# Kernel tuning notes

Measured on AMD Instinct MI355X. Metric: run time of the kernel, lower is better.

## Reference

```python
import jax, jax.numpy as jnp
import numpy as np

WIN_LEN = 400
WIN_INC = 100
FFT_LEN = 512
EPSILON = float(np.finfo(np.float32).eps)


def _make_kernel():
    # periodic (fftbins=True) hamming window, matching scipy.signal.get_window
    n = np.arange(WIN_LEN)
    window = 0.54 - 0.46 * np.cos(2.0 * np.pi * n / WIN_LEN)
    # direct-DFT basis: rfft of identity, truncated to win_len taps
    fourier_basis = np.fft.rfft(np.eye(FFT_LEN))[:WIN_LEN]          # [win_len, fft_len//2+1]
    kernel = np.concatenate([fourier_basis.real, fourier_basis.imag], axis=1).T  # [2*(fft//2+1), win_len]
    kernel = kernel * window                                        # window applied per tap
    return kernel[:, None, :].astype(np.float32)                    # [514, 1, 400] (OIH)


def setup_inputs() -> dict:
    key = jax.random.key(0)
    inputs = jax.random.normal(key, (16, 160000), dtype=jnp.float32)  # [B, L] waveform
    weight = jnp.asarray(_make_kernel())                              # fixed DFT buffer
    return {"inputs": inputs, "weight": weight}


def reference(inputs, weight):
    pad = WIN_LEN - WIN_INC  # 300
    x = inputs[:, None, :]                                   # [B, 1, L]
    x = jnp.pad(x, ((0, 0), (0, 0), (pad, pad)))             # symmetric pad, as in F.pad
    out = jax.lax.conv_general_dilated(
        x, weight,
        window_strides=(WIN_INC,),
        padding='VALID',
        dimension_numbers=('NCH', 'OIH', 'NCH'),
    )                                                        # [B, 514, T]
    r, i = jnp.split(out, 2, axis=1)                         # real / imag halves [B, 257, T]
    mags = jnp.sqrt(jnp.clip(r * r + i * i, EPSILON))
    phase = jnp.arctan2(i + EPSILON, r + EPSILON)
    return mags, phase
```

## Files before the change

### kernel.cpp

```cpp
#include <hip/hip_runtime.h>
#include <math.h>


#define BATCH 16
#define NSAMP 160000
#define NF 257
#define NT 1603
#define KLEN 400
#define INC 100
#define PADL 300
#define EPSF 1.1920928955078125e-7f
#define TAU 1e-2f

#define FPB 16
#define ZSTR 258
#define XSPAN ((FPB - 1) * INC + KLEN)
#define NTB ((NT + FPB - 1) / FPB)

__device__ __forceinline__ float2 cmul(float2 a, float2 b) {
  return make_float2(a.x * b.x - a.y * b.y, a.x * b.y + a.y * b.x);
}

__device__ __forceinline__ void fft16_dif(float2* a) {
  const float C1 = 0.92387953251128674f;
  const float S1 = 0.38268343236508978f;
  const float R2 = 0.70710678118654752f;
  {
    const float2 W[8] = {{1.f, 0.f},  {C1, -S1},  {R2, -R2},  {S1, -C1},
                         {0.f, -1.f}, {-S1, -C1}, {-R2, -R2}, {-C1, -S1}};
    #pragma unroll
    for (int j = 0; j < 8; ++j) {
      float2 u = a[j], v = a[j + 8];
      a[j] = make_float2(u.x + v.x, u.y + v.y);
      float2 d = make_float2(u.x - v.x, u.y - v.y);
      a[j + 8] = cmul(d, W[j]);
    }
  }
  {
    const float2 W[4] = {{1.f, 0.f}, {R2, -R2}, {0.f, -1.f}, {-R2, -R2}};
    #pragma unroll
    for (int h = 0; h < 16; h += 8)
      #pragma unroll
      for (int j = 0; j < 4; ++j) {
        float2 u = a[h + j], v = a[h + j + 4];
        a[h + j] = make_float2(u.x + v.x, u.y + v.y);
        float2 d = make_float2(u.x - v.x, u.y - v.y);
        a[h + j + 4] = cmul(d, W[j]);
      }
  }
  #pragma unroll
  for (int q = 0; q < 16; q += 4) {
    float2 u0 = a[q], v0 = a[q + 2];
    a[q] = make_float2(u0.x + v0.x, u0.y + v0.y);
    a[q + 2] = make_float2(u0.x - v0.x, u0.y - v0.y);
    float2 u1 = a[q + 1], v1 = a[q + 3];
    a[q + 1] = make_float2(u1.x + v1.x, u1.y + v1.y);
    float2 d = make_float2(u1.x - v1.x, u1.y - v1.y);
    a[q + 3] = make_float2(d.y, -d.x);
  }
  #pragma unroll
  for (int q = 0; q < 16; q += 2) {
    float2 u = a[q], v = a[q + 1];
    a[q] = make_float2(u.x + v.x, u.y + v.y);
    a[q + 1] = make_float2(u.x - v.x, u.y - v.y);
  }
}

__device__ __forceinline__ void emit_fp(float rr, float ii, int ff,
                                        const float* __restrict__ w,
                                        const float* xf,
                                        float* __restrict__ out,
                                        long o, long plane) {
  float ie = ii + EPSF, re = rr + EPSF;
  if (fabsf(ie) < TAU && re < TAU) {
    const float* wr = w + (long)ff * KLEN;
    const float* wi = w + (long)(257 + ff) * KLEN;
    float r2 = 0.f, i2 = 0.f;
    for (int k = 0; k < KLEN; ++k) {
      float xv = xf[k];
      r2 = fmaf(wr[k], xv, r2);
      i2 = fmaf(wi[k], xv, i2);
    }
    rr = r2; ii = i2;
  }
  out[o] = sqrtf(fmaxf(rr * rr + ii * ii, EPSF));
  out[o + plane] = atan2f(ii + EPSF, rr + EPSF);
}

__global__ __launch_bounds__(256, 3)
void stft_fft4(const float* __restrict__ x, const float* __restrict__ w,
               float* __restrict__ out) {
  __shared__ float2 Z[FPB * ZSTR];
  __shared__ float2 tw[132];
  __shared__ float2 tw256[256];
  __shared__ __align__(16) float xs[XSPAN];
  __shared__ __align__(16) float win[KLEN];

  const int tid = threadIdx.x;
  const int t0 = blockIdx.x * FPB;
  const int b = blockIdx.y;
  const int tl = tid & 15;
  const int th = tid >> 4;

  const long xb = (long)b * NSAMP;
  const int base = t0 * INC - PADL;
  for (int r = 0; r < 2; ++r) {
    int i4 = r * 256 + tid;
    if (4 * i4 < XSPAN) {
      int g = base + 4 * i4;
      float4 v;
      if (g >= 0 && g + 3 < NSAMP) {
        v = *(const float4*)(x + xb + g);
      } else {
        v.x = (g + 0 >= 0 && g + 0 < NSAMP) ? x[xb + g + 0] : 0.f;
        v.y = (g + 1 >= 0 && g + 1 < NSAMP) ? x[xb + g + 1] : 0.f;
        v.z = (g + 2 >= 0 && g + 2 < NSAMP) ? x[xb + g + 2] : 0.f;
        v.w = (g + 3 >= 0 && g + 3 < NSAMP) ? x[xb + g + 3] : 0.f;
      }
      *(float4*)&xs[4 * i4] = v;
    }
  }
  if (tid < KLEN / 4) {
    *(float4*)&win[4 * tid] = *(const float4*)(w + 4 * tid);
  }
  {
    double a = (double)tid * (6.283185307179586476925286766559 / 256.0);
    tw256[tid] = make_float2((float)cos(a), (float)(-sin(a)));
  }
  if (tid < 132) {
    double a = (double)tid * (6.283185307179586476925286766559 / 512.0);
    tw[tid] = make_float2((float)cos(a), (float)(-sin(a)));
  }
  __syncthreads();

  float2 a[16];
  const float* xf = &xs[tl * INC];
  #pragma unroll
  for (int n1 = 0; n1 < 12; ++n1) {
    int n = 32 * n1 + 2 * th;
    float2 xv = *(const float2*)&xf[n];
    float2 wv = *(const float2*)&win[n];
    a[n1] = make_float2(xv.x * wv.x, xv.y * wv.y);
  }
  {
    int n = 384 + 2 * th;
    if (n < KLEN) {
      float2 xv = *(const float2*)&xf[n];
      float2 wv = *(const float2*)&win[n];
      a[12] = make_float2(xv.x * wv.x, xv.y * wv.y);
    } else {
      a[12] = make_float2(0.f, 0.f);
    }
  }
  a[13] = a[14] = a[15] = make_float2(0.f, 0.f);

  fft16_dif(a);

  static const int BR[16] = {0, 8, 4, 12, 2, 10, 6, 14,
                             1, 9, 5, 13, 3, 11, 7, 15};
  float2* Zf = Z + tl * ZSTR;
  #pragma unroll
  for (int r = 0; r < 16; ++r) {
    const int k1 = BR[r];
    float2 v = (k1 == 0) ? a[r] : cmul(a[r], tw256[th * k1]);
    Zf[th * 16 + k1] = v;
  }
  __syncthreads();

  float2 g[16];
  #pragma unroll
  for (int n2 = 0; n2 < 16; ++n2) g[n2] = Zf[n2 * 16 + th];
  fft16_dif(g);
  #pragma unroll
  for (int r = 0; r < 16; ++r) {
    const int k2 = BR[r];
    Zf[16 * k2 + th] = g[r];
  }
  __syncthreads();

  const long plane = (long)BATCH * NF * NT;
  const long pb = (long)b * NF * NT;
  for (int r = 0; r < 9; ++r) {
    int tau = r * 256 + tid;
    if (tau < FPB * 129) {
      int t = tau & 15;
      int p = tau >> 4;
      float2* Zt = Z + t * ZSTR;
      float2 z0 = Zt[p];
      float2 z1 = Zt[(256 - p) & 255];
      float2 ze = make_float2(0.5f * (z0.x + z1.x), 0.5f * (z0.y - z1.y));
      float2 zo = make_float2(0.5f * (z0.y + z1.y), 0.5f * (z1.x - z0.x));
      float2 T = tw[p];
      float2 tz = cmul(zo, T);
      float2 ya = make_float2(ze.x + tz.x, ze.y + tz.y);
      float2 yb = make_float2(ze.x - tz.x, tz.y - ze.y);
      int tt = t0 + t;
      if (tt < NT) {
        const float* xfr = &xs[t * INC];
        emit_fp(ya.x, ya.y, p, w, xfr, out, pb + (long)p * NT + tt, plane);
        if (p == 0) {
          emit_fp(yb.x, 0.f, 256, w, xfr, out, pb + (long)256 * NT + tt, plane);
        } else {
          emit_fp(yb.x, yb.y, 256 - p, w, xfr, out,
                  pb + (long)(256 - p) * NT + tt, plane);
        }
      }
    }
  }
}

extern "C" void kernel_launch(void* const* d_in, const int* in_sizes, int n_in,
                              void* d_out, int out_size, void* d_ws, size_t ws_size,
                              hipStream_t stream) {
  const float* x = (const float*)d_in[0];
  const float* w = (const float*)d_in[1];
  float* out = (float*)d_out;

  dim3 grid(NTB, BATCH);
  stft_fft4<<<grid, dim3(256), 0, stream>>>(x, w, out);
}
```

Measured before the change: 156.0 us.

## Drop shared input staging, add fast atan2, swizzle LDS, remap blocks across XCDs

The input waveform is no longer staged in shared memory. Windowed samples are read straight from global memory, which cuts LDS use and raises the launch-bounds occupancy target from 3 to 4. The software atan2f is replaced by a polynomial approximation built on the hardware reciprocal. FFT scratch accesses use a rotated slot index to avoid LDS bank conflicts. Twiddles are computed with cospif/sinpif in float instead of double, and block indices are remapped so contiguous time tiles land on the same XCD. The polynomial atan2 adds approximation error near the tolerance boundary, and the direct global reads rely on caching for reuse across overlapping frames.

```diff
diff --git a/kernel.cpp b/kernel.cpp
--- a/kernel.cpp
+++ b/kernel.cpp
@@ -14,8 +14,8 @@
 
 #define FPB 16
 #define ZSTR 258
-#define XSPAN ((FPB - 1) * INC + KLEN)
 #define NTB ((NT + FPB - 1) / FPB)
+#define SLOT(j, k) (16 * (j) + (((k) + (j)) & 15))
 
 __device__ __forceinline__ float2 cmul(float2 a, float2 b) {
   return make_float2(a.x * b.x - a.y * b.y, a.x * b.y + a.y * b.x);
@@ -66,9 +66,26 @@
   }
 }
 
+__device__ __forceinline__ float fast_atan2(float y, float x) {
+  float ax = fabsf(x), ay = fabsf(y);
+  float mx = fmaxf(ax, ay), mn = fminf(ax, ay);
+  float t = mn * __builtin_amdgcn_rcpf(fmaxf(mx, 1e-37f));
+  float s = t * t;
+  float p = fmaf(s, -0.01172120f, 0.05265332f);
+  p = fmaf(s, p, -0.11643287f);
+  p = fmaf(s, p, 0.19354346f);
+  p = fmaf(s, p, -0.33262347f);
+  p = fmaf(s, p, 0.99997726f);
+  float r = t * p;
+  if (ay > ax) r = 1.57079632679489662f - r;
+  if (x < 0.f) r = 3.14159265358979324f - r;
+  return (y < 0.f) ? -r : r;
+}
+
 __device__ __forceinline__ void emit_fp(float rr, float ii, int ff,
                                         const float* __restrict__ w,
-                                        const float* xf,
+                                        const float* __restrict__ x,
+                                        long xb, int gb,
                                         float* __restrict__ out,
                                         long o, long plane) {
   float ie = ii + EPSF, re = rr + EPSF;
@@ -77,80 +94,64 @@
     const float* wi = w + (long)(257 + ff) * KLEN;
     float r2 = 0.f, i2 = 0.f;
     for (int k = 0; k < KLEN; ++k) {
-      float xv = xf[k];
+      int g = gb + k;
+      float xv = (g >= 0 && g < NSAMP) ? x[xb + g] : 0.f;
       r2 = fmaf(wr[k], xv, r2);
       i2 = fmaf(wi[k], xv, i2);
     }
     rr = r2; ii = i2;
   }
   out[o] = sqrtf(fmaxf(rr * rr + ii * ii, EPSF));
-  out[o + plane] = atan2f(ii + EPSF, rr + EPSF);
-}
-
-__global__ __launch_bounds__(256, 3)
-void stft_fft4(const float* __restrict__ x, const float* __restrict__ w,
+  out[o + plane] = fast_atan2(ii + EPSF, rr + EPSF);
+}
+
+__global__ __launch_bounds__(256, 4)
+void stft_fft8(const float* __restrict__ x, const float* __restrict__ w,
                float* __restrict__ out) {
   __shared__ float2 Z[FPB * ZSTR];
   __shared__ float2 tw[132];
   __shared__ float2 tw256[256];
-  __shared__ __align__(16) float xs[XSPAN];
   __shared__ __align__(16) float win[KLEN];
 
   const int tid = threadIdx.x;
-  const int t0 = blockIdx.x * FPB;
   const int b = blockIdx.y;
   const int tl = tid & 15;
   const int th = tid >> 4;
 
+  const int u = blockIdx.x;
+  const int xcd = u & 7;
+  const int tb = ((xcd < 5) ? xcd * 13 : 65 + (xcd - 5) * 12) + (u >> 3);
+  const int t0 = tb * FPB;
+
   const long xb = (long)b * NSAMP;
-  const int base = t0 * INC - PADL;
-  for (int r = 0; r < 2; ++r) {
-    int i4 = r * 256 + tid;
-    if (4 * i4 < XSPAN) {
-      int g = base + 4 * i4;
-      float4 v;
-      if (g >= 0 && g + 3 < NSAMP) {
-        v = *(const float4*)(x + xb + g);
-      } else {
-        v.x = (g + 0 >= 0 && g + 0 < NSAMP) ? x[xb + g + 0] : 0.f;
-        v.y = (g + 1 >= 0 && g + 1 < NSAMP) ? x[xb + g + 1] : 0.f;
-        v.z = (g + 2 >= 0 && g + 2 < NSAMP) ? x[xb + g + 2] : 0.f;
-        v.w = (g + 3 >= 0 && g + 3 < NSAMP) ? x[xb + g + 3] : 0.f;
-      }
-      *(float4*)&xs[4 * i4] = v;
-    }
-  }
   if (tid < KLEN / 4) {
     *(float4*)&win[4 * tid] = *(const float4*)(w + 4 * tid);
   }
   {
-    double a = (double)tid * (6.283185307179586476925286766559 / 256.0);
-    tw256[tid] = make_float2((float)cos(a), (float)(-sin(a)));
+    float a = (float)tid * (1.0f / 128.0f);
+    tw256[tid] = make_float2(cospif(a), -sinpif(a));
   }
   if (tid < 132) {
-    double a = (double)tid * (6.283185307179586476925286766559 / 512.0);
-    tw[tid] = make_float2((float)cos(a), (float)(-sin(a)));
+    float a = (float)tid * (1.0f / 256.0f);
+    tw[tid] = make_float2(cospif(a), -sinpif(a));
   }
   __syncthreads();
 
   float2 a[16];
-  const float* xf = &xs[tl * INC];
-  #pragma unroll
-  for (int n1 = 0; n1 < 12; ++n1) {
+  const int gb1 = (t0 + tl) * INC - PADL;
+  #pragma unroll
+  for (int n1 = 0; n1 < 13; ++n1) {
     int n = 32 * n1 + 2 * th;
-    float2 xv = *(const float2*)&xf[n];
-    float2 wv = *(const float2*)&win[n];
-    a[n1] = make_float2(xv.x * wv.x, xv.y * wv.y);
-  }
-  {
-    int n = 384 + 2 * th;
+    float2 zv = make_float2(0.f, 0.f);
     if (n < KLEN) {
-      float2 xv = *(const float2*)&xf[n];
-      float2 wv = *(const float2*)&win[n];
-      a[12] = make_float2(xv.x * wv.x, xv.y * wv.y);
-    } else {
-      a[12] = make_float2(0.f, 0.f);
-    }
+      int g = gb1 + n;
+      if (g >= 0 && g < NSAMP) {
+        float2 xv = *(const float2*)(x + xb + g);
+        float2 wv = *(const float2*)&win[n];
+        zv = make_float2(xv.x * wv.x, xv.y * wv.y);
+      }
+    }
+    a[n1] = zv;
   }
   a[13] = a[14] = a[15] = make_float2(0.f, 0.f);
 
@@ -163,18 +164,20 @@
   for (int r = 0; r < 16; ++r) {
     const int k1 = BR[r];
     float2 v = (k1 == 0) ? a[r] : cmul(a[r], tw256[th * k1]);
-    Zf[th * 16 + k1] = v;
+    Zf[SLOT(th, k1)] = v;
   }
   __syncthreads();
 
-  float2 g[16];
-  #pragma unroll
-  for (int n2 = 0; n2 < 16; ++n2) g[n2] = Zf[n2 * 16 + th];
-  fft16_dif(g);
-  #pragma unroll
-  for (int r = 0; r < 16; ++r) {
-    const int k2 = BR[r];
-    Zf[16 * k2 + th] = g[r];
+  {
+    float2 g[16];
+    #pragma unroll
+    for (int n2 = 0; n2 < 16; ++n2) g[n2] = Zf[SLOT(n2, th)];
+    fft16_dif(g);
+    #pragma unroll
+    for (int r = 0; r < 16; ++r) {
+      const int k2 = BR[r];
+      Zf[SLOT(k2, th)] = g[r];
+    }
   }
   __syncthreads();
 
@@ -183,25 +186,28 @@
   for (int r = 0; r < 9; ++r) {
     int tau = r * 256 + tid;
     if (tau < FPB * 129) {
-      int t = tau & 15;
+      int t16 = tau & 15;
       int p = tau >> 4;
-      float2* Zt = Z + t * ZSTR;
-      float2 z0 = Zt[p];
-      float2 z1 = Zt[(256 - p) & 255];
+      float2* Zt = Z + t16 * ZSTR;
+      int q = (256 - p) & 255;
+      float2 z0 = Zt[SLOT(p >> 4, p & 15)];
+      float2 z1 = Zt[SLOT(q >> 4, q & 15)];
       float2 ze = make_float2(0.5f * (z0.x + z1.x), 0.5f * (z0.y - z1.y));
       float2 zo = make_float2(0.5f * (z0.y + z1.y), 0.5f * (z1.x - z0.x));
       float2 T = tw[p];
       float2 tz = cmul(zo, T);
       float2 ya = make_float2(ze.x + tz.x, ze.y + tz.y);
       float2 yb = make_float2(ze.x - tz.x, tz.y - ze.y);
-      int tt = t0 + t;
+      int tt = t0 + t16;
       if (tt < NT) {
-        const float* xfr = &xs[t * INC];
-        emit_fp(ya.x, ya.y, p, w, xfr, out, pb + (long)p * NT + tt, plane);
+        int gbt = tt * INC - PADL;
+        emit_fp(ya.x, ya.y, p, w, x, xb, gbt, out,
+                pb + (long)p * NT + tt, plane);
         if (p == 0) {
-          emit_fp(yb.x, 0.f, 256, w, xfr, out, pb + (long)256 * NT + tt, plane);
+          emit_fp(yb.x, 0.f, 256, w, x, xb, gbt, out,
+                  pb + (long)256 * NT + tt, plane);
         } else {
-          emit_fp(yb.x, yb.y, 256 - p, w, xfr, out,
+          emit_fp(yb.x, yb.y, 256 - p, w, x, xb, gbt, out,
                   pb + (long)(256 - p) * NT + tt, plane);
         }
       }
@@ -217,5 +223,5 @@
   float* out = (float*)d_out;
 
   dim3 grid(NTB, BATCH);
-  stft_fft4<<<grid, dim3(256), 0, stream>>>(x, w, out);
-}
+  stft_fft8<<<grid, dim3(256), 0, stream>>>(x, w, out);
+}
```

After: 265.9 us. 70.4% more time.
